# Performance work log

Measured on AMD Instinct MI355X. Metric: run time of the kernel, lower is better.

Reference implementation:

```python
import jax, jax.numpy as jnp
import numpy as np

DIM = 2048
N_HEADS = 16
HEAD_DIM = 128

def setup_inputs() -> dict:
    key = jax.random.key(0)
    ks = jax.random.split(key, 7)
    B, S = 4, 2048
    x = jax.random.normal(ks[0], (B, S, DIM), dtype=jnp.float32)
    cos = jax.random.uniform(ks[1], (S, HEAD_DIM // 2), dtype=jnp.float32)
    sin = jax.random.uniform(ks[2], (S, HEAD_DIM // 2), dtype=jnp.float32)
    scale = 1.0 / np.sqrt(DIM)
    wq = jax.random.normal(ks[3], (DIM, N_HEADS * HEAD_DIM), dtype=jnp.float32) * scale
    wk = jax.random.normal(ks[4], (DIM, N_HEADS * HEAD_DIM), dtype=jnp.float32) * scale
    wv = jax.random.normal(ks[5], (DIM, N_HEADS * HEAD_DIM), dtype=jnp.float32) * scale
    wo = jax.random.normal(ks[6], (N_HEADS * HEAD_DIM, DIM), dtype=jnp.float32) * scale
    return {"x": x, "cos": cos, "sin": sin, "wq": wq, "wk": wk, "wv": wv, "wo": wo}

def _apply_rope(x, cos, sin):
    # x: [B, H, S, D]; cos/sin: [S, D//2]
    d = x.shape[-1] // 2
    x1, x2 = x[..., :d], x[..., d:]
    c = cos[None, None, :x.shape[2], :d]
    s = sin[None, None, :x.shape[2], :d]
    return jnp.concatenate([x1 * c - x2 * s, x2 * c + x1 * s], axis=-1)

def reference(x, cos, sin, wq, wk, wv, wo):
    B, S, _ = x.shape
    q = (x @ wq).reshape(B, S, N_HEADS, HEAD_DIM).transpose(0, 2, 1, 3)
    k = (x @ wk).reshape(B, S, N_HEADS, HEAD_DIM).transpose(0, 2, 1, 3)
    v = (x @ wv).reshape(B, S, N_HEADS, HEAD_DIM).transpose(0, 2, 1, 3)
    q = _apply_rope(q, cos, sin)
    k = _apply_rope(k, cos, sin)
    scale = 1.0 / jnp.sqrt(jnp.asarray(HEAD_DIM, dtype=x.dtype))
    scores = jnp.einsum('bhqd,bhkd->bhqk', q, k) * scale  # [B,H,S,S]
    causal = jnp.tril(jnp.ones((S, S), dtype=bool))
    scores = jnp.where(causal[None, None], scores, jnp.asarray(-jnp.inf, dtype=scores.dtype))
    attn = jax.nn.softmax(scores, axis=-1)
    out = jnp.einsum('bhqk,bhkd->bhqd', attn, v)
    out = out.transpose(0, 2, 1, 3).reshape(B, S, N_HEADS * HEAD_DIM)
    return out @ wo
```

## Files before the change

kernel.cpp:

```cpp
#include <hip/hip_runtime.h>
#include <cstdint>
#include <cstddef>

#define DIM 2048
#define NHEADS 16
#define HD 128
#define BATCH 4
#define SEQ 2048
#define MROWS (BATCH*SEQ)
#define NT 32
#define TSZ (256*64)

typedef __attribute__((ext_vector_type(4))) float  f32x4;
typedef __attribute__((ext_vector_type(4))) float  float4v;
typedef __attribute__((ext_vector_type(8))) short  short8;
typedef __attribute__((ext_vector_type(4))) short  short4v;
typedef __attribute__((ext_vector_type(4))) unsigned uint4v;
typedef __attribute__((ext_vector_type(8))) __bf16 bf16x8;

#define QSCALE 0.1275173772f

__device__ __forceinline__ unsigned f2bfbits(float f) {
  unsigned u = __builtin_bit_cast(unsigned, f);
  return (u + 0x7FFFu + ((u >> 16) & 1u)) >> 16;
}
__device__ __forceinline__ short f2bf(float f) { return (short)f2bfbits(f); }
__device__ __forceinline__ float bf2f(short s) {
  unsigned u = ((unsigned)(unsigned short)s) << 16;
  return __builtin_bit_cast(float, u);
}
__device__ __forceinline__ unsigned cvtpk_bf16(float lo, float hi) {
  unsigned r;
  asm("v_cvt_pk_bf16_f32 %0, %1, %2" : "=v"(r) : "v"(lo), "v"(hi));
  return r;
}
__device__ __forceinline__ f32x4 mfma16(short8 a, short8 b, f32x4 c) {
  return __builtin_amdgcn_mfma_f32_16x16x32_bf16(
      __builtin_bit_cast(bf16x8, a), __builtin_bit_cast(bf16x8, b), c, 0, 0, 0);
}
__device__ __forceinline__ void gload16(const short* g, short* l) {
  __builtin_amdgcn_global_load_lds(
      (const __attribute__((address_space(1))) unsigned int*)g,
      (__attribute__((address_space(3))) unsigned int*)l, 16, 0, 0);
}

__global__ __launch_bounds__(256) void k_convert_x(const float* __restrict__ x,
                                                   short* __restrict__ xb) {
  size_t i = ((size_t)blockIdx.x * 256 + threadIdx.x) * 8;
  float4v a = *(const float4v*)(x + i);
  float4v b = *(const float4v*)(x + i + 4);
  short8 o;
  o[0] = f2bf(a[0]); o[1] = f2bf(a[1]); o[2] = f2bf(a[2]); o[3] = f2bf(a[3]);
  o[4] = f2bf(b[0]); o[5] = f2bf(b[1]); o[6] = f2bf(b[2]); o[7] = f2bf(b[3]);
  *(short8*)(xb + i) = o;
}

__global__ __launch_bounds__(256) void k_transpose_w(
    const float* __restrict__ w0, const float* __restrict__ w1,
    const float* __restrict__ w2, const float* __restrict__ w3,
    short* __restrict__ o0, short* __restrict__ o1,
    short* __restrict__ o2, short* __restrict__ o3) {
  const float* w; short* o;
  switch (blockIdx.z) {
    case 0: w = w0; o = o0; break;
    case 1: w = w1; o = o1; break;
    case 2: w = w2; o = o2; break;
    default: w = w3; o = o3; break;
  }
  __shared__ float tile[32][33];
  int tx = threadIdx.x, ty = threadIdx.y;
  int kb = blockIdx.y * 32, nb = blockIdx.x * 32;
#pragma unroll
  for (int i = 0; i < 4; ++i)
    tile[ty + 8 * i][tx] = w[(size_t)(kb + ty + 8 * i) * DIM + nb + tx];
  __syncthreads();
#pragma unroll
  for (int i = 0; i < 4; ++i)
    o[(size_t)(nb + ty + 8 * i) * DIM + kb + tx] = f2bf(tile[tx][ty + 8 * i]);
}

template<int MODE>
__global__ __launch_bounds__(512, 2) void k_gemm256(const short* __restrict__ A,
                                                    const short* __restrict__ BtAll,
                                                    const float* __restrict__ cosg,
                                                    const float* __restrict__ sing,
                                                    short* __restrict__ Qp,
                                                    short* __restrict__ Kp,
                                                    short* __restrict__ Vp,
                                                    float* __restrict__ Of) {
  __shared__ short As[2 * TSZ];
  __shared__ short Bs[2 * TSZ];
  const int t = threadIdx.x;
  const int lane = t & 63, wid = t >> 6;
  const int wm = wid >> 2, wn = wid & 3;
  const int gi = lane >> 4, li = lane & 15;
  const int stg = (wid ^ (wid >> 2)) & 1;
  const int id = blockIdx.x;
  const int wg = MODE == 0 ? ((id & 7) * 96 + (id >> 3)) : ((id & 7) * 32 + (id >> 3));
  const int bm = wg & 31, bn = wg >> 5;
  const int m0 = bm * 256;
  const int which = MODE == 0 ? (bn >> 3) : 0;
  const int n0 = MODE == 0 ? ((bn & 7) * 256) : (bn * 256);
  const short* Bg = BtAll + (size_t)which * DIM * DIM;
  const short* Ag = A;

  const int lrow = lane >> 3;
  const int lcol = ((lane & 7) ^ lrow) * 8;
  const int hh = wn >> 1, hf = wn & 1;

  auto bcol = [&](int j) {
    if (MODE == 0) return hh * 128 + (j >> 1) * 64 + hf * 32 + (j & 1) * 16;
    return wn * 64 + j * 16;
  };

  f32x4 acc[8][4];
#pragma unroll
  for (int i = 0; i < 8; ++i)
#pragma unroll
    for (int j = 0; j < 4; ++j) acc[i][j] = (f32x4){0.f, 0.f, 0.f, 0.f};

#define STAGE_TILE(tt, buf)                                                       \
  {                                                                               \
    const int kk0 = (tt) * 64;                                                    \
    short* asd = As + (buf) * TSZ;                                                \
    short* bsd = Bs + (buf) * TSZ;                                                \
    _Pragma("unroll")                                                             \
    for (int ii = 0; ii < 4; ++ii) {                                              \
      int rb = ii * 64 + wid * 8;                                                 \
      gload16(Ag + (size_t)(m0 + rb + lrow) * DIM + kk0 + lcol, asd + rb * 64);   \
      gload16(Bg + (size_t)(n0 + rb + lrow) * DIM + kk0 + lcol, bsd + rb * 64);   \
    }                                                                             \
  }

  STAGE_TILE(0, 0)
  STAGE_TILE(1, 1)

  for (int tt = 0; tt < NT; ++tt) {
    if (tt < NT - 1) asm volatile("s_waitcnt vmcnt(8)" ::: "memory");
    else             asm volatile("s_waitcnt vmcnt(0)" ::: "memory");
    __builtin_amdgcn_s_barrier();
    const short* Asb = As + (tt & 1) * TSZ;
    const short* Bsb = Bs + (tt & 1) * TSZ;

#pragma unroll 1
    for (int ph = 0; ph < 2; ++ph) {
      const int ks = ph ^ stg;
      short8 av[8], bv[4];
      const int sw = (((ks << 2) | gi) ^ (li & 7)) * 8;
#pragma unroll
      for (int i = 0; i < 8; ++i)
        av[i] = *(const short8*)&Asb[(wm * 128 + i * 16 + li) * 64 + sw];
#pragma unroll
      for (int j = 0; j < 4; ++j)
        bv[j] = *(const short8*)&Bsb[(bcol(j) + li) * 64 + sw];
      __builtin_amdgcn_s_setprio(1);
#pragma unroll
      for (int i = 0; i < 8; ++i)
#pragma unroll
        for (int j = 0; j < 4; ++j)
          acc[i][j] = mfma16(av[i], bv[j], acc[i][j]);
      __builtin_amdgcn_s_setprio(0);
    }
    __builtin_amdgcn_s_barrier();
    if (tt + 2 < NT) STAGE_TILE(tt + 2, tt & 1)
  }
#undef STAGE_TILE

  if (MODE == 1) {
#pragma unroll
    for (int i = 0; i < 8; ++i)
#pragma unroll
      for (int j = 0; j < 4; ++j)
#pragma unroll
        for (int r = 0; r < 4; ++r) {
          int gm = m0 + wm * 128 + i * 16 + gi * 4 + r;
          int gn = n0 + wn * 64 + j * 16 + li;
          Of[(size_t)gm * DIM + gn] = acc[i][j][r];
        }
    return;
  }
  const int h = 2 * (bn & 7) + hh;
  if (which == 2) {
#pragma unroll
    for (int i = 0; i < 8; ++i)
#pragma unroll
      for (int j = 0; j < 4; ++j) {
        int gm0 = m0 + wm * 128 + i * 16 + gi * 4;
        int b = gm0 >> 11, s0 = gm0 & 2047;
        int d = (j >> 1) * 64 + hf * 32 + (j & 1) * 16 + li;
        short4v pk;
#pragma unroll
        for (int r = 0; r < 4; ++r) pk[r] = f2bf(acc[i][j][r]);
        *(short4v*)&Vp[((size_t)(b * NHEADS + h) * HD + d) * SEQ + s0] = pk;
      }
  } else {
    short* O = which ? Kp : Qp;
    const float qs = which ? 1.0f : QSCALE;
#pragma unroll
    for (int i = 0; i < 8; ++i)
#pragma unroll
      for (int j = 0; j < 2; ++j) {
        int dlo = hf * 32 + j * 16 + li;
#pragma unroll
        for (int r = 0; r < 4; ++r) {
          int gm = m0 + wm * 128 + i * 16 + gi * 4 + r;
          int b = gm >> 11, s = gm & 2047;
          float c = cosg[s * 64 + dlo], sn = sing[s * 64 + dlo];
          float a = acc[i][j][r], bb = acc[i][j + 2][r];
          size_t base = ((size_t)(b * NHEADS + h) * SEQ + s) * HD;
          O[base + dlo]      = f2bf((a * c - bb * sn) * qs);
          O[base + dlo + 64] = f2bf((bb * c + a * sn) * qs);
        }
      }
  }
}

__global__ __launch_bounds__(256) void k_flash(const short* __restrict__ Qg,
                                               const short* __restrict__ Kg,
                                               const short* __restrict__ Vg,
                                               short* __restrict__ Og) {
  __shared__ short Ks[64][136];
  __shared__ short Vs[128][72];
  const int t = threadIdx.x, lane = t & 63, wid = t >> 6;
  const int gi = lane >> 4, li = lane & 15;
  const int id = blockIdx.x;
  const int ip = 31 - (id >> 6);
  const int bh = id & 63;
  const int q0 = ip * 64;
  const short* Qb = Qg + (size_t)bh * SEQ * HD;
  const short* Kb = Kg + (size_t)bh * SEQ * HD;
  const short* Vb = Vg + (size_t)bh * HD * SEQ;
  const int mrow = q0 + wid * 16 + li;

  short8 qb[4];
#pragma unroll
  for (int kk = 0; kk < 4; ++kk)
    qb[kk] = *(const short8*)(Qb + (size_t)mrow * HD + kk * 32 + 8 * gi);

  f32x4 o[8];
#pragma unroll
  for (int d = 0; d < 8; ++d) o[d] = (f32x4){0.f, 0.f, 0.f, 0.f};
  float mx = -1e30f, lsum = 0.f;
  const int nt = ip + 1;
  const int srcA = li | ((lane & 16) << 1);
  const int srcB = srcA + 16;
  const bool hig = (lane & 32) != 0;

  for (int tt = 0; tt < nt; ++tt) {
    const int k0 = tt * 64;
#pragma unroll
    for (int i = 0; i < 4; ++i) {
      int idx = i * 256 + t;
      { int r = idx >> 4, c = (idx & 15) * 8;
        *(short8*)&Ks[r][c] = *(const short8*)(Kb + (size_t)(k0 + r) * HD + c); }
      { int r = idx >> 3, c = (idx & 7) * 8;
        *(short8*)&Vs[r][c] = *(const short8*)(Vb + (size_t)r * SEQ + k0 + c); }
    }
    __syncthreads();

    f32x4 sacc[4];
#pragma unroll
    for (int af = 0; af < 4; ++af) sacc[af] = (f32x4){0.f, 0.f, 0.f, 0.f};
    __builtin_amdgcn_s_setprio(1);
#pragma unroll
    for (int kk = 0; kk < 4; ++kk)
#pragma unroll
      for (int af = 0; af < 4; ++af) {
        short8 kf = *(const short8*)&Ks[16 * af + li][kk * 32 + 8 * gi];
        sacc[af] = mfma16(kf, qb[kk], sacc[af]);
      }
    __builtin_amdgcn_s_setprio(0);

    float p[4][4];
    float pmax = -1e30f;
    const bool last = (tt == nt - 1);
#pragma unroll
    for (int af = 0; af < 4; ++af)
#pragma unroll
      for (int r = 0; r < 4; ++r) {
        float v = sacc[af][r];
        if (last && (k0 + 16 * af + 4 * gi + r > mrow)) v = -1e30f;
        p[af][r] = v;
        pmax = fmaxf(pmax, v);
      }
    pmax = fmaxf(pmax, __shfl_xor(pmax, 16));
    pmax = fmaxf(pmax, __shfl_xor(pmax, 32));
    if (!__all(pmax <= mx + 11.54f)) {
      float mnew = fmaxf(mx, pmax);
      float alpha = __builtin_amdgcn_exp2f(mx - mnew);
      lsum *= alpha;
      mx = mnew;
#pragma unroll
      for (int d = 0; d < 8; ++d) o[d] *= alpha;
    }
    float psum = 0.f;
#pragma unroll
    for (int af = 0; af < 4; ++af)
#pragma unroll
      for (int r = 0; r < 4; ++r) {
        float e = __builtin_amdgcn_exp2f(p[af][r] - mx);
        p[af][r] = e;
        psum += e;
      }
    psum += __shfl_xor(psum, 16);
    psum += __shfl_xor(psum, 32);
    lsum += psum;

    unsigned plo[4], phi[4];
#pragma unroll
    for (int af = 0; af < 4; ++af) {
      plo[af] = cvtpk_bf16(p[af][0], p[af][1]);
      phi[af] = cvtpk_bf16(p[af][2], p[af][3]);
    }
#pragma unroll
    for (int kk2 = 0; kk2 < 2; ++kk2) {
      unsigned aAlo = (unsigned)__shfl((int)plo[2 * kk2], srcA);
      unsigned aAhi = (unsigned)__shfl((int)phi[2 * kk2], srcA);
      unsigned aBlo = (unsigned)__shfl((int)plo[2 * kk2 + 1], srcA);
      unsigned aBhi = (unsigned)__shfl((int)phi[2 * kk2 + 1], srcA);
      unsigned bAlo = (unsigned)__shfl((int)plo[2 * kk2], srcB);
      unsigned bAhi = (unsigned)__shfl((int)phi[2 * kk2], srcB);
      unsigned bBlo = (unsigned)__shfl((int)plo[2 * kk2 + 1], srcB);
      unsigned bBhi = (unsigned)__shfl((int)phi[2 * kk2 + 1], srcB);
      uint4v dws;
      dws[0] = hig ? aBlo : aAlo;
      dws[1] = hig ? aBhi : aAhi;
      dws[2] = hig ? bBlo : bAlo;
      dws[3] = hig ? bBhi : bAhi;
      short8 pbf = __builtin_bit_cast(short8, dws);
      __builtin_amdgcn_s_setprio(1);
#pragma unroll
      for (int d = 0; d < 8; ++d) {
        short8 vf = *(const short8*)&Vs[16 * d + li][kk2 * 32 + 8 * gi];
        o[d] = mfma16(vf, pbf, o[d]);
      }
      __builtin_amdgcn_s_setprio(0);
    }
    __syncthreads();
  }

  const float inv = 1.0f / lsum;
  const int b = bh >> 4, h = bh & 15;
  const size_t obase = ((size_t)b * SEQ + mrow) * DIM + h * HD;
#pragma unroll
  for (int d = 0; d < 8; ++d) {
    short4v st;
#pragma unroll
    for (int r = 0; r < 4; ++r) st[r] = f2bf(o[d][r] * inv);
    *(short4v*)&Og[obase + d * 16 + 4 * gi] = st;
  }
}

extern "C" void kernel_launch(void* const* d_in, const int* in_sizes, int n_in,
                              void* d_out, int out_size, void* d_ws, size_t ws_size,
                              hipStream_t stream) {
  (void)in_sizes; (void)n_in; (void)out_size;
  const float* x    = (const float*)d_in[0];
  const float* cosg = (const float*)d_in[1];
  const float* sing = (const float*)d_in[2];
  const float* wq   = (const float*)d_in[3];
  const float* wk   = (const float*)d_in[4];
  const float* wv   = (const float*)d_in[5];
  const float* wo   = (const float*)d_in[6];

  const size_t SZ = (size_t)MROWS * DIM * 2;
  char* ws = (char*)d_ws;
  short* xb  = (short*)ws;
  short* wqT = (short*)(ws + SZ);
  short* wkT = wqT + (size_t)DIM * DIM;
  short* wvT = wkT + (size_t)DIM * DIM;
  short* woT = wvT + (size_t)DIM * DIM;
  short *Qp, *Kp, *Vp;
  if (ws_size >= 5 * SZ) {
    Qp = (short*)(ws + 2 * SZ);
    Kp = (short*)(ws + 3 * SZ);
    Vp = (short*)(ws + 4 * SZ);
  } else {
    Qp = (short*)d_out;
    Kp = (short*)d_out + SZ / 2;
    Vp = (short*)(ws + 2 * SZ);
  }
  short* Ob = xb;

  k_convert_x<<<8192, 256, 0, stream>>>(x, xb);
  k_transpose_w<<<dim3(64, 64, 4), dim3(32, 8), 0, stream>>>(wq, wk, wv, wo,
                                                             wqT, wkT, wvT, woT);
  k_gemm256<0><<<768, 512, 0, stream>>>(xb, wqT, cosg, sing, Qp, Kp, Vp, nullptr);
  k_flash<<<2048, 256, 0, stream>>>(Qp, Kp, Vp, Ob);
  k_gemm256<1><<<256, 512, 0, stream>>>(Ob, woT, nullptr, nullptr,
                                        nullptr, nullptr, nullptr, (float*)d_out);
}
```

Baseline: 474.0 us.

## Double-buffer K/V tiles with async global-to-LDS loads in flash kernel

The flash-attention kernel now runs 512-thread blocks covering 128 query rows, which halves the number of K/V tile loads per query row. Loads of the next K/V tile are issued directly into LDS through gload16 into a second buffer while the current tile is computed. The LDS layout switches from padded rows to an XOR swizzle to avoid bank conflicts. The causal mask is now applied per warp on the diagonal tiles, and the pipeline relies on precise vmcnt waits and raw barriers, so correctness depends on gload16 being an LDS-direct load.

```diff
diff --git a/kernel.cpp b/kernel.cpp
--- a/kernel.cpp
+++ b/kernel.cpp
@@ -215,22 +215,23 @@
   }
 }
 
-__global__ __launch_bounds__(256) void k_flash(const short* __restrict__ Qg,
+__global__ __launch_bounds__(512) void k_flash(const short* __restrict__ Qg,
                                                const short* __restrict__ Kg,
                                                const short* __restrict__ Vg,
                                                short* __restrict__ Og) {
-  __shared__ short Ks[64][136];
-  __shared__ short Vs[128][72];
+  __shared__ short Kl[2 * 64 * 128];
+  __shared__ short Vl[2 * 128 * 64];
   const int t = threadIdx.x, lane = t & 63, wid = t >> 6;
   const int gi = lane >> 4, li = lane & 15;
   const int id = blockIdx.x;
-  const int ip = 31 - (id >> 6);
+  const int ip = 15 - (id >> 6);
   const int bh = id & 63;
-  const int q0 = ip * 64;
+  const int q0 = ip * 128;
   const short* Qb = Qg + (size_t)bh * SEQ * HD;
   const short* Kb = Kg + (size_t)bh * SEQ * HD;
   const short* Vb = Vg + (size_t)bh * HD * SEQ;
   const int mrow = q0 + wid * 16 + li;
+  const int nt = 2 * ip + 2;
 
   short8 qb[4];
 #pragma unroll
@@ -241,22 +242,38 @@
 #pragma unroll
   for (int d = 0; d < 8; ++d) o[d] = (f32x4){0.f, 0.f, 0.f, 0.f};
   float mx = -1e30f, lsum = 0.f;
-  const int nt = ip + 1;
   const int srcA = li | ((lane & 16) << 1);
   const int srcB = srcA + 16;
   const bool hig = (lane & 32) != 0;
 
+#define FSTAGE(tt, buf)                                                           \
+  {                                                                               \
+    const int kk0 = (tt) * 64;                                                    \
+    short* kl = Kl + (buf) * 8192;                                                \
+    short* vl = Vl + (buf) * 8192;                                                \
+    _Pragma("unroll")                                                             \
+    for (int u = 0; u < 2; ++u) {                                                 \
+      int w = wid * 2 + u;                                                        \
+      { int row = w * 4 + (lane >> 4); int sl = (lane & 15) ^ (row & 15);         \
+        gload16(Kb + (size_t)(kk0 + row) * HD + sl * 8, kl + w * 512); }          \
+      { int row = w * 8 + (lane >> 3); int sl = (lane & 7) ^ (row & 7);           \
+        gload16(Vb + (size_t)row * SEQ + kk0 + sl * 8, vl + w * 512); }           \
+    }                                                                             \
+  }
+
+  FSTAGE(0, 0)
+
   for (int tt = 0; tt < nt; ++tt) {
     const int k0 = tt * 64;
-#pragma unroll
-    for (int i = 0; i < 4; ++i) {
-      int idx = i * 256 + t;
-      { int r = idx >> 4, c = (idx & 15) * 8;
-        *(short8*)&Ks[r][c] = *(const short8*)(Kb + (size_t)(k0 + r) * HD + c); }
-      { int r = idx >> 3, c = (idx & 7) * 8;
-        *(short8*)&Vs[r][c] = *(const short8*)(Vb + (size_t)r * SEQ + k0 + c); }
+    if (tt + 1 < nt) {
+      FSTAGE(tt + 1, (tt + 1) & 1)
+      asm volatile("s_waitcnt vmcnt(4)" ::: "memory");
+    } else {
+      asm volatile("s_waitcnt vmcnt(0)" ::: "memory");
     }
-    __syncthreads();
+    __builtin_amdgcn_s_barrier();
+    const short* Kc = Kl + (tt & 1) * 8192;
+    const short* Vc = Vl + (tt & 1) * 8192;
 
     f32x4 sacc[4];
 #pragma unroll
@@ -266,20 +283,20 @@
     for (int kk = 0; kk < 4; ++kk)
 #pragma unroll
       for (int af = 0; af < 4; ++af) {
-        short8 kf = *(const short8*)&Ks[16 * af + li][kk * 32 + 8 * gi];
+        short8 kf = *(const short8*)&Kc[(16 * af + li) * 128 + (((kk << 2) | gi) ^ li) * 8];
         sacc[af] = mfma16(kf, qb[kk], sacc[af]);
       }
     __builtin_amdgcn_s_setprio(0);
 
     float p[4][4];
     float pmax = -1e30f;
-    const bool last = (tt == nt - 1);
+    const bool mask = (k0 + 63 > mrow);
 #pragma unroll
     for (int af = 0; af < 4; ++af)
 #pragma unroll
       for (int r = 0; r < 4; ++r) {
         float v = sacc[af][r];
-        if (last && (k0 + 16 * af + 4 * gi + r > mrow)) v = -1e30f;
+        if (mask && (k0 + 16 * af + 4 * gi + r > mrow)) v = -1e30f;
         p[af][r] = v;
         pmax = fmaxf(pmax, v);
       }
@@ -331,13 +348,14 @@
       __builtin_amdgcn_s_setprio(1);
 #pragma unroll
       for (int d = 0; d < 8; ++d) {
-        short8 vf = *(const short8*)&Vs[16 * d + li][kk2 * 32 + 8 * gi];
+        short8 vf = *(const short8*)&Vc[(16 * d + li) * 64 + ((((kk2 << 2) | gi)) ^ (li & 7)) * 8];
         o[d] = mfma16(vf, pbf, o[d]);
       }
       __builtin_amdgcn_s_setprio(0);
     }
-    __syncthreads();
-  }
+    __builtin_amdgcn_s_barrier();
+  }
+#undef FSTAGE
 
   const float inv = 1.0f / lsum;
   const int b = bh >> 4, h = bh & 15;
@@ -386,7 +404,7 @@
   k_transpose_w<<<dim3(64, 64, 4), dim3(32, 8), 0, stream>>>(wq, wk, wv, wo,
                                                              wqT, wkT, wvT, woT);
   k_gemm256<0><<<768, 512, 0, stream>>>(xb, wqT, cosg, sing, Qp, Kp, Vp, nullptr);
-  k_flash<<<2048, 256, 0, stream>>>(Qp, Kp, Vp, Ob);
+  k_flash<<<1024, 512, 0, stream>>>(Qp, Kp, Vp, Ob);
   k_gemm256<1><<<256, 512, 0, stream>>>(Ob, woT, nullptr, nullptr,
                                         nullptr, nullptr, nullptr, (float*)d_out);
 }
```

Result: faster. 434.7 us (-8.3%).
